# Performance work log

Hardware: AMD Instinct MI355X
Metric: run time of the kernel (lower is better)

## Reference

```python
import jax, jax.numpy as jnp
import numpy as np

L, N, V = 24, 1024, 50277  # layers, d_model, vocab
F = 4 * N                   # ffn hidden


def _ln(x, w, b):
    mu = jnp.mean(x)
    var = jnp.mean(jnp.square(x - mu))
    return (x - mu) * jax.lax.rsqrt(var + 1e-5) * w + b


def setup_inputs():
    key = jax.random.key(0)
    ks = jax.random.split(key, 24)
    nrm = lambda k, shape, s=0.02: jax.random.normal(k, shape, dtype=jnp.float32) * s
    inp = {}
    inp["ctx"] = jax.random.randint(ks[0], (2,), 0, V, dtype=jnp.int32)
    state = jnp.zeros((5 * L, N), dtype=jnp.float32)
    state = state.at[4::5].set(-1e30)  # pp rows initialized to -1e30 (empty_state)
    inp["state"] = state
    inp["emb"] = nrm(ks[1], (V, N), 1.0)
    inp["ln0_w"] = jnp.ones((N,), jnp.float32)
    inp["ln0_b"] = jnp.zeros((N,), jnp.float32)
    inp["ln1_w"] = jnp.ones((L, N), jnp.float32)
    inp["ln1_b"] = jnp.zeros((L, N), jnp.float32)
    inp["att_mix_k"] = jax.random.uniform(ks[2], (L, N), dtype=jnp.float32)
    inp["att_mix_v"] = jax.random.uniform(ks[3], (L, N), dtype=jnp.float32)
    inp["att_mix_r"] = jax.random.uniform(ks[4], (L, N), dtype=jnp.float32)
    inp["time_first"] = nrm(ks[5], (L, N), 0.5)
    inp["time_decay"] = -jnp.exp(nrm(ks[6], (L, N), 0.5))  # loader applies -exp()
    inp["att_kw"] = nrm(ks[7], (L, N, N))
    inp["att_vw"] = nrm(ks[8], (L, N, N))
    inp["att_rw"] = nrm(ks[9], (L, N, N))
    inp["att_ow"] = nrm(ks[10], (L, N, N))
    inp["ln2_w"] = jnp.ones((L, N), jnp.float32)
    inp["ln2_b"] = jnp.zeros((L, N), jnp.float32)
    inp["ffn_mix_k"] = jax.random.uniform(ks[11], (L, N), dtype=jnp.float32)
    inp["ffn_mix_r"] = jax.random.uniform(ks[12], (L, N), dtype=jnp.float32)
    inp["ffn_kw"] = nrm(ks[13], (L, F, N))
    inp["ffn_vw"] = nrm(ks[14], (L, N, F))
    inp["ffn_rw"] = nrm(ks[15], (L, N, N))
    inp["lnout_w"] = jnp.ones((N,), jnp.float32)
    inp["lnout_b"] = jnp.zeros((N,), jnp.float32)
    inp["head"] = nrm(ks[16], (V, N))
    return inp


def reference(ctx, state, emb, ln0_w, ln0_b, ln1_w, ln1_b, att_mix_k, att_mix_v,
              att_mix_r, time_first, time_decay, att_kw, att_vw, att_rw, att_ow,
              ln2_w, ln2_b, ffn_mix_k, ffn_mix_r, ffn_kw, ffn_vw, ffn_rw,
              lnout_w, lnout_b, head):
    # token embedding mix of the last two tokens (RWKV_RNN.forward)
    x0 = (emb[ctx[-1]] * 4.0 + emb[ctx[-2]]) * 0.2
    x0 = _ln(x0, ln0_w, ln0_b)  # blocks.0.ln0 applied before layer 0
    st = state.reshape(L, 5, N)

    def step(x, per):
        (s, l1w, l1b, amk, amv, amr, tf, td, kw, vw, rw, ow,
         l2w, l2b, fmk, fmr, fkw, fvw, frw) = per
        # --- SA: WKV linear-attention recurrence (single token) ---
        xl = _ln(x, l1w, l1b)
        xk = xl * amk + s[1] * (1 - amk)
        xv = xl * amv + s[1] * (1 - amv)
        xr = xl * amr + s[1] * (1 - amr)
        r = jax.nn.sigmoid(rw @ xr)
        k = kw @ xk
        v = vw @ xv
        aa, bb, pp = s[2], s[3], s[4]
        ww = tf + k
        q = jnp.maximum(pp, ww)
        e1 = jnp.exp(pp - q)
        e2 = jnp.exp(ww - q)
        a = e1 * aa + e2 * v
        b = e1 * bb + e2
        ww2 = pp + td
        q2 = jnp.maximum(ww2, k)
        f1 = jnp.exp(ww2 - q2)
        f2 = jnp.exp(k - q2)
        naa = f1 * aa + f2 * v
        nbb = f1 * bb + f2
        npp = q2
        sx = x + ow @ (r * a / b)
        # --- FF: gated squared-relu channel mixing ---
        x2 = _ln(sx, l2w, l2b)
        fxk = x2 * fmk + s[0] * (1 - fmk)
        fxr = x2 * fmr + s[0] * (1 - fmr)
        r2 = jax.nn.sigmoid(frw @ fxr)
        kk = jnp.square(jax.nn.relu(fkw @ fxk))
        out = sx + r2 * (fvw @ kk)
        ns = jnp.stack([x2, xl, naa, nbb, npp])  # [5, N] new state rows
        return out, ns

    xs = (st, ln1_w, ln1_b, att_mix_k, att_mix_v, att_mix_r, time_first,
          time_decay, att_kw, att_vw, att_rw, att_ow, ln2_w, ln2_b,
          ffn_mix_k, ffn_mix_r, ffn_kw, ffn_vw, ffn_rw)
    xf, new_st = jax.lax.scan(step, x0, xs)
    logits = head @ _ln(xf, lnout_w, lnout_b)
    return logits, new_st.reshape(5 * L, N)
```

## Files before the change

kernel.cpp:

```cpp
#include <hip/hip_runtime.h>
#include <math.h>

#define N 1024
#define F 4096
#define NLAYERS 24
#define VOCAB 50277
#define GRID 256
#define BLOCK 512

#define SXACC_OFF N
#define FACC_OFF (N + 16384)
#define BAR_OFF_BYTES 135168
#define LINE 16
#define BAR_DWORDS (256 * LINE)
#define WS_CLEAR_BYTES (BAR_OFF_BYTES + BAR_DWORDS * 4)

__device__ __forceinline__ float dot4(float4 a, float4 b) {
  return fmaf(a.x, b.x, fmaf(a.y, b.y, fmaf(a.z, b.z, a.w * b.w)));
}
__device__ __forceinline__ float wred(float v) {
#pragma unroll
  for (int o = 32; o > 0; o >>= 1) v += __shfl_down(v, o, 64);
  return v;
}
__device__ __forceinline__ float bfly(float v) {
#pragma unroll
  for (int o = 1; o < 64; o <<= 1) v += __shfl_xor(v, o, 64);
  return v;
}
__device__ __forceinline__ float sigmoidf(float x) { return 1.f / (1.f + expf(-x)); }

__device__ __forceinline__ float2 ld_c2(const float* p) {
  unsigned long long u = __hip_atomic_load((const unsigned long long*)p,
                                           __ATOMIC_RELAXED, __HIP_MEMORY_SCOPE_AGENT);
  float2 f;
  f.x = __uint_as_float((unsigned)u);
  f.y = __uint_as_float((unsigned)(u >> 32));
  return f;
}
__device__ __forceinline__ void st_c(float* p, float v) {
  __hip_atomic_store(p, v, __ATOMIC_RELAXED, __HIP_MEMORY_SCOPE_AGENT);
}
__device__ __forceinline__ unsigned ld_cu(const unsigned* p) {
  return __hip_atomic_load(p, __ATOMIC_RELAXED, __HIP_MEMORY_SCOPE_AGENT);
}
__device__ __forceinline__ void st_cu(unsigned* p, unsigned v) {
  __hip_atomic_store(p, v, __ATOMIC_RELAXED, __HIP_MEMORY_SCOPE_AGENT);
}

__device__ __forceinline__ void lbar() {
  asm volatile("s_waitcnt lgkmcnt(0)" ::: "memory");
  __builtin_amdgcn_s_barrier();
}

__device__ __forceinline__ void gbar_arrive(unsigned* arr, unsigned gen, int blk,
                                            int tid) {
  asm volatile("s_waitcnt vmcnt(0) lgkmcnt(0)" ::: "memory");
  __builtin_amdgcn_s_barrier();
  if (tid == 0) st_cu(arr + blk * LINE, gen);
}
__device__ __forceinline__ void sweep_signal(const unsigned* arr, unsigned gen,
                                             int lane, unsigned* s_gen) {
  for (;;) {
    bool ok = true;
#pragma unroll
    for (int i = 0; i < 4; ++i)
      ok &= (ld_cu(arr + (lane * 4 + i) * LINE) >= gen);
    if (__all(ok)) break;
    __builtin_amdgcn_s_sleep(1);
  }
  __hip_atomic_store(s_gen, gen, __ATOMIC_RELAXED, __HIP_MEMORY_SCOPE_WORKGROUP);
}
__device__ __forceinline__ void lds_wait(const unsigned* s_gen, unsigned gen) {
  while (__hip_atomic_load(s_gen, __ATOMIC_RELAXED, __HIP_MEMORY_SCOPE_WORKGROUP) < gen)
    __builtin_amdgcn_s_sleep(1);
}

__device__ __forceinline__ void ln16(float4* q, const float* __restrict__ w,
                                     const float* __restrict__ b, int lane) {
  float s = 0.f, sq = 0.f;
#pragma unroll
  for (int k = 0; k < 4; ++k) {
    s += q[k].x + q[k].y + q[k].z + q[k].w;
    sq += dot4(q[k], q[k]);
  }
  s = bfly(s);
  sq = bfly(sq);
  float mu = s * (1.f / N);
  float rstd = rsqrtf(sq * (1.f / N) - mu * mu + 1e-5f);
#pragma unroll
  for (int k = 0; k < 4; ++k) {
    float4 w4 = ((const float4*)w)[(k << 6) + lane];
    float4 b4 = ((const float4*)b)[(k << 6) + lane];
    q[k].x = (q[k].x - mu) * rstd * w4.x + b4.x;
    q[k].y = (q[k].y - mu) * rstd * w4.y + b4.y;
    q[k].z = (q[k].z - mu) * rstd * w4.z + b4.z;
    q[k].w = (q[k].w - mu) * rstd * w4.w + b4.w;
  }
}

__device__ __forceinline__ float4 mix4(float4 a, float4 s, float4 m) {
  float4 r;
  r.x = a.x * m.x + s.x * (1.f - m.x);
  r.y = a.y * m.y + s.y * (1.f - m.y);
  r.z = a.z * m.z + s.z * (1.f - m.z);
  r.w = a.w * m.w + s.w * (1.f - m.w);
  return r;
}

__device__ __forceinline__ void wkv1(float k, float v, float r, float aa, float bb,
                                     float pp, float tf, float td, float& rab,
                                     float& naa, float& nbb, float& npp) {
  float ww = tf + k;
  float q = fmaxf(pp, ww);
  float e1 = expf(pp - q);
  float e2 = expf(ww - q);
  float a = e1 * aa + e2 * v;
  float b = e1 * bb + e2;
  rab = r * a / b;
  float ww2 = pp + td;
  float q2 = fmaxf(ww2, k);
  float f1 = expf(ww2 - q2);
  float f2 = expf(k - q2);
  naa = f1 * aa + f2 * v;
  nbb = f1 * bb + f2;
  npp = q2;
}

__global__ __launch_bounds__(BLOCK, 1) void k_rwkv(
    const int* __restrict__ ctx, const float* __restrict__ state,
    const float* __restrict__ emb, const float* __restrict__ ln0w,
    const float* __restrict__ ln0b, const float* __restrict__ ln1w,
    const float* __restrict__ ln1b, const float* __restrict__ amk,
    const float* __restrict__ amv, const float* __restrict__ amr,
    const float* __restrict__ tf, const float* __restrict__ td,
    const float* __restrict__ kw, const float* __restrict__ vw,
    const float* __restrict__ rw, const float* __restrict__ ow,
    const float* __restrict__ ln2w, const float* __restrict__ ln2b,
    const float* __restrict__ fmk, const float* __restrict__ fmr,
    const float* __restrict__ fkw, const float* __restrict__ fvw,
    const float* __restrict__ frw, const float* __restrict__ lnoutw,
    const float* __restrict__ lnoutb, const float* __restrict__ head,
    float* __restrict__ out, float* __restrict__ ws, unsigned* __restrict__ bar) {
  __shared__ __align__(16) float s_vx[N];
  __shared__ __align__(16) float s_sx[N];
  __shared__ __align__(16) float s_kk[16];
  __shared__ __align__(16) float s_ex[16];
  __shared__ unsigned s_gen;

  const int tid = threadIdx.x;
  const int lane = tid & 63;
  const int wid = tid >> 6;
  const int blk = blockIdx.x;
  const int i0 = 2 * tid;
  const size_t nn = (size_t)N * N;

  if (tid == 0) s_gen = 0;
  __syncthreads();

  float* logits = out;
  float* st_out = out + VOCAB;
  float* r2buf = ws;
  float* sxacc = ws + SXACC_OFF;
  float* facc = ws + FACC_OFF;
  unsigned genc = 0;

  const int xcd = blk & 7, sgrp = blk >> 3;
  const int jm = sgrp & 3, gg = sgrp >> 2;
  const int tt = xcd + (gg << 3);
  const int c0 = (tt << 4) + (jm << 2);

  const int rowA = c0 + (wid & 3);
  const int gk0 = (blk << 4) + wid, gk1 = gk0 + 8;
  const int rR = (blk << 2) + (wid & 3);
  const int rv0 = (tid + (blk << 2)) & (N - 1);
  const int rv1 = (rv0 + 512) & (N - 1);

  float4 pa0[4], pa1[4], pow0, pow1, pk0[4], pk1[4], pcr[4], pf0[4], pf1[4];

  {
    const float* W0 = ((wid < 4) ? kw : vw) + (size_t)rowA * N;
#pragma unroll
    for (int k = 0; k < 4; ++k) pa0[k] = ((const float4*)W0)[(k << 6) + lane];
    if (wid < 4) {
      const float* W1 = rw + (size_t)rowA * N;
#pragma unroll
      for (int k = 0; k < 4; ++k) pa1[k] = ((const float4*)W1)[(k << 6) + lane];
    }
    pow0 = *(const float4*)(ow + (size_t)rv0 * N + c0);
    pow1 = *(const float4*)(ow + (size_t)rv1 * N + c0);
  }

  for (int l = 0; l < NLAYERS; ++l) {
    const float* st_l = state + (size_t)l * 5 * N;
    float* sto = st_out + (size_t)l * 5 * N;
    const int p = l & 1;

    {
      float kaa = 0.f, kbb = 0.f, kpp = 0.f, ktf = 0.f, ktd = 0.f;
      if (tid < 4) {
        int ii = c0 + tid;
        kaa = st_l[2 * N + ii];
        kbb = st_l[3 * N + ii];
        kpp = st_l[4 * N + ii];
        ktf = tf[l * N + ii];
        ktd = td[l * N + ii];
      }
      if (tid < 32) st_c(sxacc + (1 - p) * 8192 + blk * 32 + tid, 0.f);

      float2 xin;
      if (l == 0) {
        int t1 = ctx[1], t0c = ctx[0];
        float2 e1 = ((const float2*)(emb + (size_t)t1 * N))[tid];
        float2 e0 = ((const float2*)(emb + (size_t)t0c * N))[tid];
        xin.x = (e1.x * 4.f + e0.x) * 0.2f;
        xin.y = (e1.y * 4.f + e0.y) * 0.2f;
      } else {
        float2 r22 = ld_c2(r2buf + i0);
        const float* fb = facc + (1 - p) * 8192;
        float fax = 0.f, fay = 0.f;
#pragma unroll
        for (int c = 0; c < 8; ++c) {
          float2 t2 = ld_c2(fb + c * N + i0);
          fax += t2.x;
          fay += t2.y;
        }
        xin.x = s_sx[i0] + r22.x * fax;
        xin.y = s_sx[i0 + 1] + r22.y * fay;
      }
      ((float2*)s_vx)[tid] = xin;
      lbar();
      float4 xq[4];
#pragma unroll
      for (int k = 0; k < 4; ++k) xq[k] = ((const float4*)s_vx)[(k << 6) + lane];
      if (l == 0) {
        ln16(xq, ln0w, ln0b, lane);
        lbar();
        if (wid == 1) {
#pragma unroll
          for (int k = 0; k < 4; ++k) ((float4*)s_vx)[(k << 6) + lane] = xq[k];
        }
      }
      float4 xl[4];
#pragma unroll
      for (int k = 0; k < 4; ++k) xl[k] = xq[k];
      ln16(xl, ln1w + l * N, ln1b + l * N, lane);
      if (blk == 4 && wid == 1) {
#pragma unroll
        for (int k = 0; k < 4; ++k) ((float4*)(sto + N))[(k << 6) + lane] = xl[k];
      }
      if (wid < 4) {
        float dK = 0.f, dR = 0.f;
#pragma unroll
        for (int k = 0; k < 4; ++k) {
          float4 s1 = ((const float4*)(st_l + N))[(k << 6) + lane];
          float4 mk = mix4(xl[k], s1, ((const float4*)(amk + l * N))[(k << 6) + lane]);
          float4 mr = mix4(xl[k], s1, ((const float4*)(amr + l * N))[(k << 6) + lane]);
          dK += dot4(pa0[k], mk);
          dR += dot4(pa1[k], mr);
        }
        dK = wred(dK);
        dR = wred(dR);
        if (lane == 0) {
          s_ex[wid] = dK;
          s_ex[8 + wid] = sigmoidf(dR);
        }
      } else {
        float dV = 0.f;
#pragma unroll
        for (int k = 0; k < 4; ++k) {
          float4 s1 = ((const float4*)(st_l + N))[(k << 6) + lane];
          float4 mv = mix4(xl[k], s1, ((const float4*)(amv + l * N))[(k << 6) + lane]);
          dV += dot4(pa0[k], mv);
        }
        dV = wred(dV);
        if (lane == 0) s_ex[4 + (wid & 3)] = dV;
      }
      lbar();
      if (tid < 4) {
        float kv = s_ex[tid], vv = s_ex[4 + tid], rr = s_ex[8 + tid];
        float rab, naa, nbb, npp;
        wkv1(kv, vv, rr, kaa, kbb, kpp, ktf, ktd, rab, naa, nbb, npp);
        int ii = c0 + tid;
        sto[2 * N + ii] = naa;
        sto[3 * N + ii] = nbb;
        sto[4 * N + ii] = npp;
        s_ex[12 + tid] = rab;
      }
      lbar();
      float4 rab4 = *((const float4*)(s_ex + 12));
      float* sxa = sxacc + p * 8192 + xcd * N;
      unsafeAtomicAdd(sxa + rv0, dot4(pow0, rab4));
      unsafeAtomicAdd(sxa + rv1, dot4(pow1, rab4));
    }
    gbar_arrive(bar, ++genc, blk, tid);
    {
      auto pfC = [&]() {
        const float* fkw_l = fkw + (size_t)l * F * N;
#pragma unroll
        for (int k = 0; k < 4; ++k)
          pk0[k] = ((const float4*)(fkw_l + (size_t)gk0 * N))[(k << 6) + lane];
#pragma unroll
        for (int k = 0; k < 4; ++k)
          pk1[k] = ((const float4*)(fkw_l + (size_t)gk1 * N))[(k << 6) + lane];
        if (wid >= 4) {
          const float* WR = frw + l * nn + (size_t)rR * N;
#pragma unroll
          for (int k = 0; k < 4; ++k) pcr[k] = ((const float4*)WR)[(k << 6) + lane];
        }
        const float* fvb = fvw + (size_t)l * N * F + (blk << 4);
#pragma unroll
        for (int i = 0; i < 4; ++i) pf0[i] = ((const float4*)(fvb + (size_t)rv0 * F))[i];
#pragma unroll
        for (int i = 0; i < 4; ++i) pf1[i] = ((const float4*)(fvb + (size_t)rv1 * F))[i];
      };
      if (wid == 0) {
        sweep_signal(bar, genc, lane, &s_gen);
        pfC();
      } else {
        pfC();
        lds_wait(&s_gen, genc);
      }
    }

    {
      if (tid < 32) st_c(facc + (1 - p) * 8192 + blk * 32 + tid, 0.f);
      const float* sb = sxacc + p * 8192;
      float fax = 0.f, fay = 0.f;
#pragma unroll
      for (int c = 0; c < 8; ++c) {
        float2 t2 = ld_c2(sb + c * N + i0);
        fax += t2.x;
        fay += t2.y;
      }
      float2 sx2;
      sx2.x = s_vx[i0] + fax;
      sx2.y = s_vx[i0 + 1] + fay;
      ((float2*)s_sx)[tid] = sx2;
      lbar();
      float4 x2q[4];
#pragma unroll
      for (int k = 0; k < 4; ++k) x2q[k] = ((const float4*)s_sx)[(k << 6) + lane];
      ln16(x2q, ln2w + l * N, ln2b + l * N, lane);
      if (blk == 5 && wid == 1) {
#pragma unroll
        for (int k = 0; k < 4; ++k) ((float4*)sto)[(k << 6) + lane] = x2q[k];
      }
      float4 mk[4];
#pragma unroll
      for (int k = 0; k < 4; ++k) {
        float4 s0 = ((const float4*)st_l)[(k << 6) + lane];
        mk[k] = mix4(x2q[k], s0, ((const float4*)(fmk + l * N))[(k << 6) + lane]);
      }
      float d0 = 0.f, d1 = 0.f;
#pragma unroll
      for (int k = 0; k < 4; ++k) {
        d0 += dot4(pk0[k], mk[k]);
        d1 += dot4(pk1[k], mk[k]);
      }
      d0 = wred(d0);
      d1 = wred(d1);
      if (lane == 0) {
        float t0 = fmaxf(d0, 0.f);
        s_kk[wid] = t0 * t0;
        float t1 = fmaxf(d1, 0.f);
        s_kk[8 + wid] = t1 * t1;
      }
      if (wid >= 4) {
        float dr = 0.f;
#pragma unroll
        for (int k = 0; k < 4; ++k) {
          float4 s0 = ((const float4*)st_l)[(k << 6) + lane];
          float4 mr = mix4(x2q[k], s0, ((const float4*)(fmr + l * N))[(k << 6) + lane]);
          dr += dot4(pcr[k], mr);
        }
        dr = wred(dr);
        if (lane == 0) st_c(r2buf + rR, sigmoidf(dr));
      }
      lbar();
      float4 K0 = ((const float4*)s_kk)[0];
      float4 K1 = ((const float4*)s_kk)[1];
      float4 K2 = ((const float4*)s_kk)[2];
      float4 K3 = ((const float4*)s_kk)[3];
      float* fc = facc + p * 8192 + xcd * N;
      unsafeAtomicAdd(fc + rv0, dot4(pf0[0], K0) + dot4(pf0[1], K1) +
                                    dot4(pf0[2], K2) + dot4(pf0[3], K3));
      unsafeAtomicAdd(fc + rv1, dot4(pf1[0], K0) + dot4(pf1[1], K1) +
                                    dot4(pf1[2], K2) + dot4(pf1[3], K3));
    }
    gbar_arrive(bar, ++genc, blk, tid);
    {
      auto pfA = [&]() {
        if (l + 1 < NLAYERS) {
          const float* W0 = ((wid < 4) ? kw : vw) + (l + 1) * nn + (size_t)rowA * N;
#pragma unroll
          for (int k = 0; k < 4; ++k) pa0[k] = ((const float4*)W0)[(k << 6) + lane];
          if (wid < 4) {
            const float* W1 = rw + (l + 1) * nn + (size_t)rowA * N;
#pragma unroll
            for (int k = 0; k < 4; ++k) pa1[k] = ((const float4*)W1)[(k << 6) + lane];
          }
          const float* owl = ow + (l + 1) * nn;
          pow0 = *(const float4*)(owl + (size_t)rv0 * N + c0);
          pow1 = *(const float4*)(owl + (size_t)rv1 * N + c0);
        }
      };
      if (wid == 0) {
        sweep_signal(bar, genc, lane, &s_gen);
        pfA();
      } else {
        pfA();
        lds_wait(&s_gen, genc);
      }
    }
  }

  {
    float2 r22 = ld_c2(r2buf + i0);
    const float* fb = facc + ((NLAYERS - 1) & 1) * 8192;
    float fax = 0.f, fay = 0.f;
#pragma unroll
    for (int c = 0; c < 8; ++c) {
      float2 t2 = ld_c2(fb + c * N + i0);
      fax += t2.x;
      fay += t2.y;
    }
    float2 xf2;
    xf2.x = s_sx[i0] + r22.x * fax;
    xf2.y = s_sx[i0 + 1] + r22.y * fay;
    ((float2*)s_vx)[tid] = xf2;
    lbar();
    float4 xf[4];
#pragma unroll
    for (int k = 0; k < 4; ++k) xf[k] = ((const float4*)s_vx)[(k << 6) + lane];
    ln16(xf, lnoutw, lnoutb, lane);
    int gw = (blk << 3) + wid;
    for (int base = gw * 4; base < VOCAB; base += GRID * 8 * 4) {
      float4 h[4][4];
#pragma unroll
      for (int rr = 0; rr < 4; ++rr) {
        int row = base + rr;
        if (row < VOCAB) {
          const float4* hp = (const float4*)(head + (size_t)row * N);
#pragma unroll
          for (int k = 0; k < 4; ++k) h[rr][k] = hp[(k << 6) + lane];
        }
      }
#pragma unroll
      for (int rr = 0; rr < 4; ++rr) {
        int row = base + rr;
        if (row < VOCAB) {
          float d = 0.f;
#pragma unroll
          for (int k = 0; k < 4; ++k) d += dot4(h[rr][k], xf[k]);
          d = wred(d);
          if (lane == 0) logits[row] = d;
        }
      }
    }
  }
}

extern "C" void kernel_launch(void* const* d_in, const int* in_sizes, int n_in,
                              void* d_out, int out_size, void* d_ws, size_t ws_size,
                              hipStream_t stream) {
  const int* ctx = (const int*)d_in[0];
  const float* state = (const float*)d_in[1];
  const float* emb = (const float*)d_in[2];
  const float* ln0w = (const float*)d_in[3];
  const float* ln0b = (const float*)d_in[4];
  const float* ln1w = (const float*)d_in[5];
  const float* ln1b = (const float*)d_in[6];
  const float* amk = (const float*)d_in[7];
  const float* amv = (const float*)d_in[8];
  const float* amr = (const float*)d_in[9];
  const float* tf = (const float*)d_in[10];
  const float* td = (const float*)d_in[11];
  const float* kw = (const float*)d_in[12];
  const float* vw = (const float*)d_in[13];
  const float* rw = (const float*)d_in[14];
  const float* ow = (const float*)d_in[15];
  const float* ln2w = (const float*)d_in[16];
  const float* ln2b = (const float*)d_in[17];
  const float* fmk = (const float*)d_in[18];
  const float* fmr = (const float*)d_in[19];
  const float* fkw = (const float*)d_in[20];
  const float* fvw = (const float*)d_in[21];
  const float* frw = (const float*)d_in[22];
  const float* lnoutw = (const float*)d_in[23];
  const float* lnoutb = (const float*)d_in[24];
  const float* head = (const float*)d_in[25];
  float* out = (float*)d_out;
  float* ws = (float*)d_ws;
  unsigned* bar = (unsigned*)((char*)d_ws + BAR_OFF_BYTES);

  hipMemsetAsync(d_ws, 0, WS_CLEAR_BYTES, stream);

  void* args[] = {&ctx, &state, &emb, &ln0w, &ln0b, &ln1w, &ln1b,
                  &amk, &amv, &amr, &tf, &td, &kw, &vw, &rw, &ow,
                  &ln2w, &ln2b, &fmk, &fmr, &fkw, &fvw, &frw,
                  &lnoutw, &lnoutb, &head, &out, &ws, &bar};
  hipLaunchCooperativeKernel((const void*)k_rwkv, dim3(GRID), dim3(BLOCK),
                             args, 0, stream);
}
```

Baseline: 616.5 us.

## Add dedicated ninth wave for barrier polling and WKV scalar work

Raises the block size from 512 to 576 threads so a ninth wavefront handles the grid-barrier sweep, the WKV scalar update, state loading and accumulator clearing. The eight compute waves now only prefetch weights and wait on an LDS flag, and no longer have wave 0 doing both polling and prefetch. The extra wave also joins the final head projection, which now splits rows across 9 waves per block. The cost is one more wave per block and more branching on the work flag, plus extra register and occupancy pressure from the larger block.

Result: slower. 958.4 us (+55.5%).

```diff
diff --git a/kernel.cpp b/kernel.cpp
--- a/kernel.cpp
+++ b/kernel.cpp
@@ -6,7 +6,7 @@
 #define NLAYERS 24
 #define VOCAB 50277
 #define GRID 256
-#define BLOCK 512
+#define BLOCK 576
 
 #define SXACC_OFF N
 #define FACC_OFF (N + 16384)
@@ -57,7 +57,7 @@
                                             int tid) {
   asm volatile("s_waitcnt vmcnt(0) lgkmcnt(0)" ::: "memory");
   __builtin_amdgcn_s_barrier();
-  if (tid == 0) st_cu(arr + blk * LINE, gen);
+  if (tid == 512) st_cu(arr + blk * LINE, gen);
 }
 __device__ __forceinline__ void sweep_signal(const unsigned* arr, unsigned gen,
                                              int lane, unsigned* s_gen) {
@@ -151,6 +151,7 @@
   const int tid = threadIdx.x;
   const int lane = tid & 63;
   const int wid = tid >> 6;
+  const bool work = (wid < 8);
   const int blk = blockIdx.x;
   const int i0 = 2 * tid;
   const size_t nn = (size_t)N * N;
@@ -178,7 +179,7 @@
 
   float4 pa0[4], pa1[4], pow0, pow1, pk0[4], pk1[4], pcr[4], pf0[4], pf1[4];
 
-  {
+  if (work) {
     const float* W0 = ((wid < 4) ? kw : vw) + (size_t)rowA * N;
 #pragma unroll
     for (int k = 0; k < 4; ++k) pa0[k] = ((const float4*)W0)[(k << 6) + lane];
@@ -198,244 +199,254 @@
 
     {
       float kaa = 0.f, kbb = 0.f, kpp = 0.f, ktf = 0.f, ktd = 0.f;
-      if (tid < 4) {
-        int ii = c0 + tid;
-        kaa = st_l[2 * N + ii];
-        kbb = st_l[3 * N + ii];
-        kpp = st_l[4 * N + ii];
-        ktf = tf[l * N + ii];
-        ktd = td[l * N + ii];
-      }
-      if (tid < 32) st_c(sxacc + (1 - p) * 8192 + blk * 32 + tid, 0.f);
-
-      float2 xin;
+      if (!work) {
+        int sl = tid - 512;
+        if (sl < 4) {
+          int ii = c0 + sl;
+          kaa = st_l[2 * N + ii];
+          kbb = st_l[3 * N + ii];
+          kpp = st_l[4 * N + ii];
+          ktf = tf[l * N + ii];
+          ktd = td[l * N + ii];
+        }
+        if (sl < 32) st_c(sxacc + (1 - p) * 8192 + blk * 32 + sl, 0.f);
+      } else {
+        float2 xin;
+        if (l == 0) {
+          int t1 = ctx[1], t0c = ctx[0];
+          float2 e1 = ((const float2*)(emb + (size_t)t1 * N))[tid];
+          float2 e0 = ((const float2*)(emb + (size_t)t0c * N))[tid];
+          xin.x = (e1.x * 4.f + e0.x) * 0.2f;
+          xin.y = (e1.y * 4.f + e0.y) * 0.2f;
+        } else {
+          float2 r22 = ld_c2(r2buf + i0);
+          const float* fb = facc + (1 - p) * 8192;
+          float fax = 0.f, fay = 0.f;
+#pragma unroll
+          for (int c = 0; c < 8; ++c) {
+            float2 t2 = ld_c2(fb + c * N + i0);
+            fax += t2.x;
+            fay += t2.y;
+          }
+          xin.x = s_sx[i0] + r22.x * fax;
+          xin.y = s_sx[i0 + 1] + r22.y * fay;
+        }
+        ((float2*)s_vx)[tid] = xin;
+      }
+      lbar();
+      float4 xq[4];
+      if (work) {
+#pragma unroll
+        for (int k = 0; k < 4; ++k) xq[k] = ((const float4*)s_vx)[(k << 6) + lane];
+      }
       if (l == 0) {
-        int t1 = ctx[1], t0c = ctx[0];
-        float2 e1 = ((const float2*)(emb + (size_t)t1 * N))[tid];
-        float2 e0 = ((const float2*)(emb + (size_t)t0c * N))[tid];
-        xin.x = (e1.x * 4.f + e0.x) * 0.2f;
-        xin.y = (e1.y * 4.f + e0.y) * 0.2f;
+        if (work) ln16(xq, ln0w, ln0b, lane);
+        lbar();
+        if (wid == 1) {
+#pragma unroll
+          for (int k = 0; k < 4; ++k) ((float4*)s_vx)[(k << 6) + lane] = xq[k];
+        }
+      }
+      if (work) {
+        float4 xl[4];
+#pragma unroll
+        for (int k = 0; k < 4; ++k) xl[k] = xq[k];
+        ln16(xl, ln1w + l * N, ln1b + l * N, lane);
+        if (blk == 4 && wid == 1) {
+#pragma unroll
+          for (int k = 0; k < 4; ++k) ((float4*)(sto + N))[(k << 6) + lane] = xl[k];
+        }
+        if (wid < 4) {
+          float dK = 0.f, dR = 0.f;
+#pragma unroll
+          for (int k = 0; k < 4; ++k) {
+            float4 s1 = ((const float4*)(st_l + N))[(k << 6) + lane];
+            float4 mk = mix4(xl[k], s1, ((const float4*)(amk + l * N))[(k << 6) + lane]);
+            float4 mr = mix4(xl[k], s1, ((const float4*)(amr + l * N))[(k << 6) + lane]);
+            dK += dot4(pa0[k], mk);
+            dR += dot4(pa1[k], mr);
+          }
+          dK = wred(dK);
+          dR = wred(dR);
+          if (lane == 0) {
+            s_ex[wid] = dK;
+            s_ex[8 + wid] = sigmoidf(dR);
+          }
+        } else {
+          float dV = 0.f;
+#pragma unroll
+          for (int k = 0; k < 4; ++k) {
+            float4 s1 = ((const float4*)(st_l + N))[(k << 6) + lane];
+            float4 mv = mix4(xl[k], s1, ((const float4*)(amv + l * N))[(k << 6) + lane]);
+            dV += dot4(pa0[k], mv);
+          }
+          dV = wred(dV);
+          if (lane == 0) s_ex[4 + (wid & 3)] = dV;
+        }
+      }
+      lbar();
+      if (!work) {
+        int sl = tid - 512;
+        if (sl < 4) {
+          float kv = s_ex[sl], vv = s_ex[4 + sl], rr = s_ex[8 + sl];
+          float rab, naa, nbb, npp;
+          wkv1(kv, vv, rr, kaa, kbb, kpp, ktf, ktd, rab, naa, nbb, npp);
+          int ii = c0 + sl;
+          sto[2 * N + ii] = naa;
+          sto[3 * N + ii] = nbb;
+          sto[4 * N + ii] = npp;
+          s_ex[12 + sl] = rab;
+        }
+      }
+      lbar();
+      if (work) {
+        float4 rab4 = *((const float4*)(s_ex + 12));
+        float* sxa = sxacc + p * 8192 + xcd * N;
+        unsafeAtomicAdd(sxa + rv0, dot4(pow0, rab4));
+        unsafeAtomicAdd(sxa + rv1, dot4(pow1, rab4));
+      }
+    }
+    gbar_arrive(bar, ++genc, blk, tid);
+    if (!work) {
+      sweep_signal(bar, genc, lane, &s_gen);
+    } else {
+      const float* fkw_l = fkw + (size_t)l * F * N;
+#pragma unroll
+      for (int k = 0; k < 4; ++k)
+        pk0[k] = ((const float4*)(fkw_l + (size_t)gk0 * N))[(k << 6) + lane];
+#pragma unroll
+      for (int k = 0; k < 4; ++k)
+        pk1[k] = ((const float4*)(fkw_l + (size_t)gk1 * N))[(k << 6) + lane];
+      if (wid >= 4) {
+        const float* WR = frw + l * nn + (size_t)rR * N;
+#pragma unroll
+        for (int k = 0; k < 4; ++k) pcr[k] = ((const float4*)WR)[(k << 6) + lane];
+      }
+      const float* fvb = fvw + (size_t)l * N * F + (blk << 4);
+#pragma unroll
+      for (int i = 0; i < 4; ++i) pf0[i] = ((const float4*)(fvb + (size_t)rv0 * F))[i];
+#pragma unroll
+      for (int i = 0; i < 4; ++i) pf1[i] = ((const float4*)(fvb + (size_t)rv1 * F))[i];
+      lds_wait(&s_gen, genc);
+    }
+
+    {
+      if (!work) {
+        int sl = tid - 512;
+        if (sl < 32) st_c(facc + (1 - p) * 8192 + blk * 32 + sl, 0.f);
       } else {
-        float2 r22 = ld_c2(r2buf + i0);
-        const float* fb = facc + (1 - p) * 8192;
+        const float* sb = sxacc + p * 8192;
         float fax = 0.f, fay = 0.f;
 #pragma unroll
         for (int c = 0; c < 8; ++c) {
-          float2 t2 = ld_c2(fb + c * N + i0);
+          float2 t2 = ld_c2(sb + c * N + i0);
           fax += t2.x;
           fay += t2.y;
         }
-        xin.x = s_sx[i0] + r22.x * fax;
-        xin.y = s_sx[i0 + 1] + r22.y * fay;
-      }
-      ((float2*)s_vx)[tid] = xin;
+        float2 sx2;
+        sx2.x = s_vx[i0] + fax;
+        sx2.y = s_vx[i0 + 1] + fay;
+        ((float2*)s_sx)[tid] = sx2;
+      }
       lbar();
-      float4 xq[4];
-#pragma unroll
-      for (int k = 0; k < 4; ++k) xq[k] = ((const float4*)s_vx)[(k << 6) + lane];
-      if (l == 0) {
-        ln16(xq, ln0w, ln0b, lane);
-        lbar();
-        if (wid == 1) {
-#pragma unroll
-          for (int k = 0; k < 4; ++k) ((float4*)s_vx)[(k << 6) + lane] = xq[k];
-        }
-      }
-      float4 xl[4];
-#pragma unroll
-      for (int k = 0; k < 4; ++k) xl[k] = xq[k];
-      ln16(xl, ln1w + l * N, ln1b + l * N, lane);
-      if (blk == 4 && wid == 1) {
-#pragma unroll
-        for (int k = 0; k < 4; ++k) ((float4*)(sto + N))[(k << 6) + lane] = xl[k];
-      }
-      if (wid < 4) {
-        float dK = 0.f, dR = 0.f;
+      if (work) {
+        float4 x2q[4];
+#pragma unroll
+        for (int k = 0; k < 4; ++k) x2q[k] = ((const float4*)s_sx)[(k << 6) + lane];
+        ln16(x2q, ln2w + l * N, ln2b + l * N, lane);
+        if (blk == 5 && wid == 1) {
+#pragma unroll
+          for (int k = 0; k < 4; ++k) ((float4*)sto)[(k << 6) + lane] = x2q[k];
+        }
+        float4 mk[4];
 #pragma unroll
         for (int k = 0; k < 4; ++k) {
-          float4 s1 = ((const float4*)(st_l + N))[(k << 6) + lane];
-          float4 mk = mix4(xl[k], s1, ((const float4*)(amk + l * N))[(k << 6) + lane]);
-          float4 mr = mix4(xl[k], s1, ((const float4*)(amr + l * N))[(k << 6) + lane]);
-          dK += dot4(pa0[k], mk);
-          dR += dot4(pa1[k], mr);
-        }
-        dK = wred(dK);
-        dR = wred(dR);
+          float4 s0 = ((const float4*)st_l)[(k << 6) + lane];
+          mk[k] = mix4(x2q[k], s0, ((const float4*)(fmk + l * N))[(k << 6) + lane]);
+        }
+        float d0 = 0.f, d1 = 0.f;
+#pragma unroll
+        for (int k = 0; k < 4; ++k) {
+          d0 += dot4(pk0[k], mk[k]);
+          d1 += dot4(pk1[k], mk[k]);
+        }
+        d0 = wred(d0);
+        d1 = wred(d1);
         if (lane == 0) {
-          s_ex[wid] = dK;
-          s_ex[8 + wid] = sigmoidf(dR);
-        }
-      } else {
-        float dV = 0.f;
-#pragma unroll
-        for (int k = 0; k < 4; ++k) {
-          float4 s1 = ((const float4*)(st_l + N))[(k << 6) + lane];
-          float4 mv = mix4(xl[k], s1, ((const float4*)(amv + l * N))[(k << 6) + lane]);
-          dV += dot4(pa0[k], mv);
-        }
-        dV = wred(dV);
-        if (lane == 0) s_ex[4 + (wid & 3)] = dV;
+          float t0 = fmaxf(d0, 0.f);
+          s_kk[wid] = t0 * t0;
+          float t1 = fmaxf(d1, 0.f);
+          s_kk[8 + wid] = t1 * t1;
+        }
+        if (wid >= 4) {
+          float dr = 0.f;
+#pragma unroll
+          for (int k = 0; k < 4; ++k) {
+            float4 s0 = ((const float4*)st_l)[(k << 6) + lane];
+            float4 mr = mix4(x2q[k], s0, ((const float4*)(fmr + l * N))[(k << 6) + lane]);
+            dr += dot4(pcr[k], mr);
+          }
+          dr = wred(dr);
+          if (lane == 0) st_c(r2buf + rR, sigmoidf(dr));
+        }
       }
       lbar();
-      if (tid < 4) {
-        float kv = s_ex[tid], vv = s_ex[4 + tid], rr = s_ex[8 + tid];
-        float rab, naa, nbb, npp;
-        wkv1(kv, vv, rr, kaa, kbb, kpp, ktf, ktd, rab, naa, nbb, npp);
-        int ii = c0 + tid;
-        sto[2 * N + ii] = naa;
-        sto[3 * N + ii] = nbb;
-        sto[4 * N + ii] = npp;
-        s_ex[12 + tid] = rab;
-      }
-      lbar();
-      float4 rab4 = *((const float4*)(s_ex + 12));
-      float* sxa = sxacc + p * 8192 + xcd * N;
-      unsafeAtomicAdd(sxa + rv0, dot4(pow0, rab4));
-      unsafeAtomicAdd(sxa + rv1, dot4(pow1, rab4));
+      if (work) {
+        float4 K0 = ((const float4*)s_kk)[0];
+        float4 K1 = ((const float4*)s_kk)[1];
+        float4 K2 = ((const float4*)s_kk)[2];
+        float4 K3 = ((const float4*)s_kk)[3];
+        float* fc = facc + p * 8192 + xcd * N;
+        unsafeAtomicAdd(fc + rv0, dot4(pf0[0], K0) + dot4(pf0[1], K1) +
+                                      dot4(pf0[2], K2) + dot4(pf0[3], K3));
+        unsafeAtomicAdd(fc + rv1, dot4(pf1[0], K0) + dot4(pf1[1], K1) +
+                                      dot4(pf1[2], K2) + dot4(pf1[3], K3));
+      }
     }
     gbar_arrive(bar, ++genc, blk, tid);
-    {
-      auto pfC = [&]() {
-        const float* fkw_l = fkw + (size_t)l * F * N;
-#pragma unroll
-        for (int k = 0; k < 4; ++k)
-          pk0[k] = ((const float4*)(fkw_l + (size_t)gk0 * N))[(k << 6) + lane];
-#pragma unroll
-        for (int k = 0; k < 4; ++k)
-          pk1[k] = ((const float4*)(fkw_l + (size_t)gk1 * N))[(k << 6) + lane];
-        if (wid >= 4) {
-          const float* WR = frw + l * nn + (size_t)rR * N;
-#pragma unroll
-          for (int k = 0; k < 4; ++k) pcr[k] = ((const float4*)WR)[(k << 6) + lane];
-        }
-        const float* fvb = fvw + (size_t)l * N * F + (blk << 4);
-#pragma unroll
-        for (int i = 0; i < 4; ++i) pf0[i] = ((const float4*)(fvb + (size_t)rv0 * F))[i];
-#pragma unroll
-        for (int i = 0; i < 4; ++i) pf1[i] = ((const float4*)(fvb + (size_t)rv1 * F))[i];
-      };
-      if (wid == 0) {
-        sweep_signal(bar, genc, lane, &s_gen);
-        pfC();
-      } else {
-        pfC();
-        lds_wait(&s_gen, genc);
-      }
-    }
-
-    {
-      if (tid < 32) st_c(facc + (1 - p) * 8192 + blk * 32 + tid, 0.f);
-      const float* sb = sxacc + p * 8192;
+    if (!work) {
+      sweep_signal(bar, genc, lane, &s_gen);
+    } else {
+      if (l + 1 < NLAYERS) {
+        const float* W0 = ((wid < 4) ? kw : vw) + (l + 1) * nn + (size_t)rowA * N;
+#pragma unroll
+        for (int k = 0; k < 4; ++k) pa0[k] = ((const float4*)W0)[(k << 6) + lane];
+        if (wid < 4) {
+          const float* W1 = rw + (l + 1) * nn + (size_t)rowA * N;
+#pragma unroll
+          for (int k = 0; k < 4; ++k) pa1[k] = ((const float4*)W1)[(k << 6) + lane];
+        }
+        const float* owl = ow + (l + 1) * nn;
+        pow0 = *(const float4*)(owl + (size_t)rv0 * N + c0);
+        pow1 = *(const float4*)(owl + (size_t)rv1 * N + c0);
+      }
+      lds_wait(&s_gen, genc);
+    }
+  }
+
+  {
+    if (work) {
+      float2 r22 = ld_c2(r2buf + i0);
+      const float* fb = facc + ((NLAYERS - 1) & 1) * 8192;
       float fax = 0.f, fay = 0.f;
 #pragma unroll
       for (int c = 0; c < 8; ++c) {
-        float2 t2 = ld_c2(sb + c * N + i0);
+        float2 t2 = ld_c2(fb + c * N + i0);
         fax += t2.x;
         fay += t2.y;
       }
-      float2 sx2;
-      sx2.x = s_vx[i0] + fax;
-      sx2.y = s_vx[i0 + 1] + fay;
-      ((float2*)s_sx)[tid] = sx2;
-      lbar();
-      float4 x2q[4];
-#pragma unroll
-      for (int k = 0; k < 4; ++k) x2q[k] = ((const float4*)s_sx)[(k << 6) + lane];
-      ln16(x2q, ln2w + l * N, ln2b + l * N, lane);
-      if (blk == 5 && wid == 1) {
-#pragma unroll
-        for (int k = 0; k < 4; ++k) ((float4*)sto)[(k << 6) + lane] = x2q[k];
-      }
-      float4 mk[4];
-#pragma unroll
-      for (int k = 0; k < 4; ++k) {
-        float4 s0 = ((const float4*)st_l)[(k << 6) + lane];
-        mk[k] = mix4(x2q[k], s0, ((const float4*)(fmk + l * N))[(k << 6) + lane]);
-      }
-      float d0 = 0.f, d1 = 0.f;
-#pragma unroll
-      for (int k = 0; k < 4; ++k) {
-        d0 += dot4(pk0[k], mk[k]);
-        d1 += dot4(pk1[k], mk[k]);
-      }
-      d0 = wred(d0);
-      d1 = wred(d1);
-      if (lane == 0) {
-        float t0 = fmaxf(d0, 0.f);
-        s_kk[wid] = t0 * t0;
-        float t1 = fmaxf(d1, 0.f);
-        s_kk[8 + wid] = t1 * t1;
-      }
-      if (wid >= 4) {
-        float dr = 0.f;
-#pragma unroll
-        for (int k = 0; k < 4; ++k) {
-          float4 s0 = ((const float4*)st_l)[(k << 6) + lane];
-          float4 mr = mix4(x2q[k], s0, ((const float4*)(fmr + l * N))[(k << 6) + lane]);
-          dr += dot4(pcr[k], mr);
-        }
-        dr = wred(dr);
-        if (lane == 0) st_c(r2buf + rR, sigmoidf(dr));
-      }
-      lbar();
-      float4 K0 = ((const float4*)s_kk)[0];
-      float4 K1 = ((const float4*)s_kk)[1];
-      float4 K2 = ((const float4*)s_kk)[2];
-      float4 K3 = ((const float4*)s_kk)[3];
-      float* fc = facc + p * 8192 + xcd * N;
-      unsafeAtomicAdd(fc + rv0, dot4(pf0[0], K0) + dot4(pf0[1], K1) +
-                                    dot4(pf0[2], K2) + dot4(pf0[3], K3));
-      unsafeAtomicAdd(fc + rv1, dot4(pf1[0], K0) + dot4(pf1[1], K1) +
-                                    dot4(pf1[2], K2) + dot4(pf1[3], K3));
-    }
-    gbar_arrive(bar, ++genc, blk, tid);
-    {
-      auto pfA = [&]() {
-        if (l + 1 < NLAYERS) {
-          const float* W0 = ((wid < 4) ? kw : vw) + (l + 1) * nn + (size_t)rowA * N;
-#pragma unroll
-          for (int k = 0; k < 4; ++k) pa0[k] = ((const float4*)W0)[(k << 6) + lane];
-          if (wid < 4) {
-            const float* W1 = rw + (l + 1) * nn + (size_t)rowA * N;
-#pragma unroll
-            for (int k = 0; k < 4; ++k) pa1[k] = ((const float4*)W1)[(k << 6) + lane];
-          }
-          const float* owl = ow + (l + 1) * nn;
-          pow0 = *(const float4*)(owl + (size_t)rv0 * N + c0);
-          pow1 = *(const float4*)(owl + (size_t)rv1 * N + c0);
-        }
-      };
-      if (wid == 0) {
-        sweep_signal(bar, genc, lane, &s_gen);
-        pfA();
-      } else {
-        pfA();
-        lds_wait(&s_gen, genc);
-      }
-    }
-  }
-
-  {
-    float2 r22 = ld_c2(r2buf + i0);
-    const float* fb = facc + ((NLAYERS - 1) & 1) * 8192;
-    float fax = 0.f, fay = 0.f;
-#pragma unroll
-    for (int c = 0; c < 8; ++c) {
-      float2 t2 = ld_c2(fb + c * N + i0);
-      fax += t2.x;
-      fay += t2.y;
-    }
-    float2 xf2;
-    xf2.x = s_sx[i0] + r22.x * fax;
-    xf2.y = s_sx[i0 + 1] + r22.y * fay;
-    ((float2*)s_vx)[tid] = xf2;
+      float2 xf2;
+      xf2.x = s_sx[i0] + r22.x * fax;
+      xf2.y = s_sx[i0 + 1] + r22.y * fay;
+      ((float2*)s_vx)[tid] = xf2;
+    }
     lbar();
     float4 xf[4];
 #pragma unroll
     for (int k = 0; k < 4; ++k) xf[k] = ((const float4*)s_vx)[(k << 6) + lane];
     ln16(xf, lnoutw, lnoutb, lane);
-    int gw = (blk << 3) + wid;
-    for (int base = gw * 4; base < VOCAB; base += GRID * 8 * 4) {
+    int gw = blk * 9 + wid;
+    for (int base = gw * 4; base < VOCAB; base += GRID * 9 * 4) {
       float4 h[4][4];
 #pragma unroll
       for (int rr = 0; rr < 4; ++rr) {
```
